# Optimization experiments

Hardware: AMD Instinct MI355X
Metric: run time of the kernel (lower is better)

## Reference

```python
import jax, jax.numpy as jnp
import numpy as np

EMBED = 1024
HEADS = 16
HEAD_DIM = EMBED // HEADS
GROUP_SIZE = 64
NUM_GROUPS = EMBED // GROUP_SIZE
BATCH, SEQ = 2, 2048


def dequantize(qw, scales, zeros):
    # qw: [O, I] int, scales/zeros: [O, NUM_GROUPS]
    O, I = qw.shape
    w = qw.reshape(O, NUM_GROUPS, GROUP_SIZE).astype(scales.dtype)
    w = (w - zeros[:, :, None]) * scales[:, :, None]
    return w.reshape(O, I)


def setup_inputs() -> dict:
    key = jax.random.key(0)
    ks = jax.random.split(key, 17)
    d = {"hidden_states": jax.random.normal(ks[0], (BATCH, SEQ, EMBED), jnp.float32)}
    i = 1
    for p in ("q", "k", "v", "o"):
        d[f"{p}_qw"] = jax.random.randint(ks[i], (EMBED, EMBED), 0, 127, jnp.int32)
        d[f"{p}_scales"] = jax.random.uniform(ks[i + 1], (EMBED, NUM_GROUPS), jnp.float32) * 0.01 + 1e-4
        d[f"{p}_zeros"] = jax.random.uniform(ks[i + 2], (EMBED, NUM_GROUPS), jnp.float32) * 64.0
        d[f"{p}_bias"] = jax.random.normal(ks[i + 3], (EMBED,), jnp.float32) * 0.01
        i += 4
    return d


def reference(hidden_states,
              q_qw, q_scales, q_zeros, q_bias,
              k_qw, k_scales, k_zeros, k_bias,
              v_qw, v_scales, v_zeros, v_bias,
              o_qw, o_scales, o_zeros, o_bias):
    B, S, E = hidden_states.shape

    def proj(x, qw, s, z, b):
        w = dequantize(qw, s, z)  # [O, I]
        return jnp.einsum('bse,oe->bso', x, w) + b

    # [B, S, E] -> [B, H, S, D]
    def split_heads(t):
        return t.reshape(B, S, HEADS, HEAD_DIM).transpose(0, 2, 1, 3)

    q = split_heads(proj(hidden_states, q_qw, q_scales, q_zeros, q_bias))
    k = split_heads(proj(hidden_states, k_qw, k_scales, k_zeros, k_bias))
    v = split_heads(proj(hidden_states, v_qw, v_scales, v_zeros, v_bias))

    scores = jnp.einsum('bhsd,bhtd->bhst', q, k) / (HEAD_DIM ** 0.5)
    attn_weights = jax.nn.softmax(scores, axis=-1)
    attn_out = jnp.einsum('bhst,bhtd->bhsd', attn_weights, v)
    attn_out = attn_out.transpose(0, 2, 1, 3).reshape(B, S, E)

    output = proj(attn_out, o_qw, o_scales, o_zeros, o_bias)
    return output, attn_weights
```

## Files before the change

kernel.cpp:

```cpp
#include <hip/hip_runtime.h>
#include <math.h>

#define EMB 1024
#define NH 16
#define HD 64
#define NB 2
#define SQ 2048
#define BSQ (NB*SQ)
#define NG 16
#define OUT0 ((size_t)BSQ*EMB)

typedef __attribute__((ext_vector_type(8))) short bf16x8;
typedef __attribute__((ext_vector_type(4))) float f32x4;

__device__ __forceinline__ short f2bf(float x){
    unsigned u = __float_as_uint(x);
    u += 0x7fff + ((u >> 16) & 1);
    return (short)(u >> 16);
}
__device__ __forceinline__ float bf2f(short h){
    return __uint_as_float(((unsigned)(unsigned short)h) << 16);
}

__global__ __launch_bounds__(256) void prep_w(
        const int* qq, const float* qs, const float* qz,
        const int* kq, const float* ks, const float* kz,
        const int* vq, const float* vs, const float* vz,
        const int* oq, const float* os, const float* oz,
        short* __restrict__ Wh, short* __restrict__ Wl)
{
    int z = blockIdx.z;
    const int*   qw = z==0?qq : z==1?kq : z==2?vq : oq;
    const float* sc = z==0?qs : z==1?ks : z==2?vs : os;
    const float* zp = z==0?qz : z==1?kz : z==2?vz : oz;
    size_t base = (size_t)z*EMB*EMB;
    int idx = (blockIdx.x*256 + threadIdx.x)*8;
    int4 a = *(const int4*)(qw + idx);
    int4 b = *(const int4*)(qw + idx + 4);
    int o = idx >> 10, g = (idx & 1023) >> 6;
    float s = sc[o*NG + g], zv = zp[o*NG + g];
    int qv[8] = {a.x,a.y,a.z,a.w,b.x,b.y,b.z,b.w};
    alignas(16) short hv[8];
    alignas(16) short lv[8];
    #pragma unroll
    for (int j = 0; j < 8; ++j) {
        float wv = ((float)qv[j] - zv)*s;
        short h = f2bf(wv); hv[j] = h;
        lv[j] = f2bf(wv - bf2f(h));
    }
    *(bf16x8*)(Wh + base + idx) = *(const bf16x8*)hv;
    if (z < 2)
        *(bf16x8*)(Wl + base + idx) = *(const bf16x8*)lv;
}

__global__ __launch_bounds__(256) void prep_x(
        const float* __restrict__ X, short* __restrict__ Xh, short* __restrict__ Xl)
{
    int idx = (blockIdx.x*256 + threadIdx.x)*8;
    float4 a = *(const float4*)(X + idx);
    float4 b = *(const float4*)(X + idx + 4);
    float xv[8] = {a.x,a.y,a.z,a.w,b.x,b.y,b.z,b.w};
    alignas(16) short hv[8];
    alignas(16) short lv[8];
    #pragma unroll
    for (int j = 0; j < 8; ++j) {
        short h = f2bf(xv[j]); hv[j] = h;
        lv[j] = f2bf(xv[j] - bf2f(h));
    }
    *(bf16x8*)(Xh + idx) = *(const bf16x8*)hv;
    *(bf16x8*)(Xl + idx) = *(const bf16x8*)lv;
}

template<int TERMS, int EPI>
__global__ __launch_bounds__(256, 2) void k_proj(
        const short* __restrict__ Ahg, const short* __restrict__ Alg,
        const short* __restrict__ Bhg, const short* __restrict__ Blg,
        const float* __restrict__ bias,
        short* __restrict__ outH, short* __restrict__ outL,
        float* __restrict__ outF)
{
    constexpr bool SPL = (TERMS > 1);
    constexpr int LSTR = 40;
    constexpr int MSZ  = 128*LSTR*(SPL?2:1);
    constexpr int STAGE = 2*MSZ;
    constexpr int TSH  = (EPI == 3) ? 128*136 : 0;
    constexpr int LDSN = (STAGE > TSH) ? STAGE : TSH;
    __shared__ short lds[LDSN];
    short* As  = lds;
    short* Bs  = lds + MSZ;
    short* Asl = As + 128*LSTR;
    short* Bsl = Bs + 128*LSTR;

    const int tid = threadIdx.x;
    const int l = tid & 63, w = tid >> 6;
    const int lrow = l & 15, lq = l >> 4;
    const int wr = w >> 1, wc = w & 1;
    const int m0 = blockIdx.y*128, n0 = blockIdx.x*128;
    const int r = tid >> 1, kh = (tid & 1)*16;

    f32x4 acc[4][4] = {};

    for (int k0 = 0; k0 < EMB; k0 += 32) {
        const short* as = Ahg + (size_t)(m0 + r)*EMB + k0 + kh;
        bf16x8 a0 = *(const bf16x8*)as;
        bf16x8 a1 = *(const bf16x8*)(as + 8);
        const short* bs = Bhg + (size_t)(n0 + r)*EMB + k0 + kh;
        bf16x8 b0 = *(const bf16x8*)bs;
        bf16x8 b1 = *(const bf16x8*)(bs + 8);
        bf16x8 a2{}, a3{}, b2{}, b3{};
        if constexpr (SPL) {
            const short* as2 = Alg + (size_t)(m0 + r)*EMB + k0 + kh;
            a2 = *(const bf16x8*)as2; a3 = *(const bf16x8*)(as2 + 8);
            const short* bs2 = Blg + (size_t)(n0 + r)*EMB + k0 + kh;
            b2 = *(const bf16x8*)bs2; b3 = *(const bf16x8*)(bs2 + 8);
        }
        __syncthreads();
        *(bf16x8*)(As + r*LSTR + kh)     = a0;
        *(bf16x8*)(As + r*LSTR + kh + 8) = a1;
        *(bf16x8*)(Bs + r*LSTR + kh)     = b0;
        *(bf16x8*)(Bs + r*LSTR + kh + 8) = b1;
        if constexpr (SPL) {
            *(bf16x8*)(Asl + r*LSTR + kh)     = a2;
            *(bf16x8*)(Asl + r*LSTR + kh + 8) = a3;
            *(bf16x8*)(Bsl + r*LSTR + kh)     = b2;
            *(bf16x8*)(Bsl + r*LSTR + kh + 8) = b3;
        }
        __syncthreads();

        bf16x8 aH[4], aL[4], bH[4], bL[4];
        #pragma unroll
        for (int i = 0; i < 4; ++i) {
            aH[i] = *(const bf16x8*)(As + (wr*64 + i*16 + lrow)*LSTR + lq*8);
            if constexpr (SPL) aL[i] = *(const bf16x8*)(Asl + (wr*64 + i*16 + lrow)*LSTR + lq*8);
        }
        #pragma unroll
        for (int j = 0; j < 4; ++j) {
            bH[j] = *(const bf16x8*)(Bs + (wc*64 + j*16 + lrow)*LSTR + lq*8);
            if constexpr (SPL) bL[j] = *(const bf16x8*)(Bsl + (wc*64 + j*16 + lrow)*LSTR + lq*8);
        }
        #pragma unroll
        for (int i = 0; i < 4; ++i)
            #pragma unroll
            for (int j = 0; j < 4; ++j) {
                acc[i][j] = __builtin_amdgcn_mfma_f32_16x16x32_bf16(aH[i], bH[j], acc[i][j], 0, 0, 0);
                if constexpr (SPL) {
                    acc[i][j] = __builtin_amdgcn_mfma_f32_16x16x32_bf16(aH[i], bL[j], acc[i][j], 0, 0, 0);
                    acc[i][j] = __builtin_amdgcn_mfma_f32_16x16x32_bf16(aL[i], bH[j], acc[i][j], 0, 0, 0);
                }
            }
    }

    if constexpr (EPI == 3) {
        __syncthreads();
        #pragma unroll
        for (int i = 0; i < 4; ++i) {
            int rl = wr*64 + i*16 + lq*4;
            #pragma unroll
            for (int j = 0; j < 4; ++j) {
                int cl = wc*64 + j*16 + lrow;
                float bv = bias[n0 + cl];
                #pragma unroll
                for (int rr = 0; rr < 4; ++rr)
                    lds[cl*136 + rl + rr] = f2bf(acc[i][j][rr] + bv);
            }
        }
        __syncthreads();
        int c = tid >> 1, hf = (tid & 1)*64;
        int gc = n0 + c;
        int z2 = (m0 >> 11)*16 + (gc >> 6);
        int d = gc & 63;
        short* dst = outH + ((size_t)z2*HD + d)*SQ + (m0 & (SQ-1)) + hf;
        #pragma unroll
        for (int u = 0; u < 8; ++u)
            *(bf16x8*)(dst + u*8) = *(const bf16x8*)(lds + c*136 + hf + u*8);
        return;
    }

    #pragma unroll
    for (int i = 0; i < 4; ++i) {
        int rb = m0 + wr*64 + i*16 + lq*4;
        #pragma unroll
        for (int j = 0; j < 4; ++j) {
            int cb = n0 + wc*64 + j*16 + lrow;
            float bv = bias[cb];
            #pragma unroll
            for (int rr = 0; rr < 4; ++rr) {
                float y = acc[i][j][rr] + bv;
                size_t off = (size_t)(rb + rr)*EMB + cb;
                if constexpr (EPI == 0) {
                    short hh = f2bf(y);
                    outH[off] = hh;
                    outL[off] = f2bf(y - bf2f(hh));
                } else {
                    outF[off] = y;
                }
            }
        }
    }
}

template<int PASS>
__global__ __launch_bounds__(256, 2) void k_attn(
        const short* __restrict__ Qh, const short* __restrict__ Ql,
        const short* __restrict__ Kh, const short* __restrict__ Kl,
        const short* __restrict__ Vt,
        float* __restrict__ ml,
        float* __restrict__ attn,
        short* __restrict__ AO)
{
    constexpr int LSTR = 72;
    __shared__ short qbuf[128*LSTR*2];
    __shared__ short kbuf[64*LSTR*2];
    __shared__ short vbuf[(PASS==2) ? 64*LSTR : 8];
    constexpr int QOFF = 128*LSTR;
    constexpr int KOFF = 64*LSTR;

    const int tid = threadIdx.x;
    const int l = tid & 63, w = tid >> 6;
    const int lrow = l & 15, lq = l >> 4;
    const int z = blockIdx.y, b = z >> 4, h = z & 15;
    const int i0 = blockIdx.x*128;
    const size_t qrow0 = (size_t)(b*SQ + i0);
    const size_t zbase = (size_t)z*SQ*SQ;

    {
        int rr = tid >> 1, kh2 = (tid & 1)*32;
        const short* qh = Qh + (qrow0 + rr)*EMB + h*HD + kh2;
        const short* ql = Ql + (qrow0 + rr)*EMB + h*HD + kh2;
        #pragma unroll
        for (int u = 0; u < 4; ++u) {
            *(bf16x8*)(qbuf + rr*LSTR + kh2 + u*8)        = *(const bf16x8*)(qh + u*8);
            *(bf16x8*)(qbuf + QOFF + rr*LSTR + kh2 + u*8) = *(const bf16x8*)(ql + u*8);
        }
    }
    __syncthreads();
    bf16x8 aH[2][2], aL[2][2];
    #pragma unroll
    for (int i = 0; i < 2; ++i)
        #pragma unroll
        for (int ks = 0; ks < 2; ++ks) {
            aH[i][ks] = *(const bf16x8*)(qbuf + (w*32 + i*16 + lrow)*LSTR + ks*32 + lq*8);
            aL[i][ks] = *(const bf16x8*)(qbuf + QOFF + (w*32 + i*16 + lrow)*LSTR + ks*32 + lq*8);
        }

    float m_st[2][4], l_st[2][4];
    #pragma unroll
    for (int i = 0; i < 2; ++i)
        #pragma unroll
        for (int rr = 0; rr < 4; ++rr) {
            if constexpr (PASS == 1) {
                m_st[i][rr] = -INFINITY; l_st[i][rr] = 0.f;
            } else {
                int row = i0 + w*32 + i*16 + lq*4 + rr;
                m_st[i][rr] = ml[(size_t)z*SQ + row];
                l_st[i][rr] = 1.0f / ml[(size_t)NB*NH*SQ + (size_t)z*SQ + row];
            }
        }

    f32x4 oa[2][4] = {};

    for (int j0 = 0; j0 < SQ; j0 += 64) {
        int c = tid >> 2, kh2 = (tid & 3)*16;
        const short* khp = Kh + (size_t)(b*SQ + j0 + c)*EMB + h*HD + kh2;
        const short* klp = Kl + (size_t)(b*SQ + j0 + c)*EMB + h*HD + kh2;
        bf16x8 k0a = *(const bf16x8*)khp;
        bf16x8 k0b = *(const bf16x8*)(khp + 8);
        bf16x8 k1a = *(const bf16x8*)klp;
        bf16x8 k1b = *(const bf16x8*)(klp + 8);
        bf16x8 va{}, vb{};
        if constexpr (PASS == 2) {
            const short* vp = Vt + ((size_t)z*HD + c)*SQ + j0 + kh2;
            va = *(const bf16x8*)vp;
            vb = *(const bf16x8*)(vp + 8);
        }
        __syncthreads();
        *(bf16x8*)(kbuf + c*LSTR + kh2)            = k0a;
        *(bf16x8*)(kbuf + c*LSTR + kh2 + 8)        = k0b;
        *(bf16x8*)(kbuf + KOFF + c*LSTR + kh2)     = k1a;
        *(bf16x8*)(kbuf + KOFF + c*LSTR + kh2 + 8) = k1b;
        if constexpr (PASS == 2) {
            *(bf16x8*)(vbuf + c*LSTR + kh2)     = va;
            *(bf16x8*)(vbuf + c*LSTR + kh2 + 8) = vb;
        }
        __syncthreads();

        f32x4 acc[2][4] = {};
        #pragma unroll
        for (int ks = 0; ks < 2; ++ks) {
            bf16x8 bH[4], bL[4];
            #pragma unroll
            for (int jj = 0; jj < 4; ++jj) {
                bH[jj] = *(const bf16x8*)(kbuf + (jj*16 + lrow)*LSTR + ks*32 + lq*8);
                bL[jj] = *(const bf16x8*)(kbuf + KOFF + (jj*16 + lrow)*LSTR + ks*32 + lq*8);
            }
            #pragma unroll
            for (int i = 0; i < 2; ++i)
                #pragma unroll
                for (int jj = 0; jj < 4; ++jj) {
                    acc[i][jj] = __builtin_amdgcn_mfma_f32_16x16x32_bf16(aH[i][ks], bH[jj], acc[i][jj], 0, 0, 0);
                    acc[i][jj] = __builtin_amdgcn_mfma_f32_16x16x32_bf16(aH[i][ks], bL[jj], acc[i][jj], 0, 0, 0);
                    acc[i][jj] = __builtin_amdgcn_mfma_f32_16x16x32_bf16(aL[i][ks], bH[jj], acc[i][jj], 0, 0, 0);
                }
        }

        #pragma unroll
        for (int i = 0; i < 2; ++i)
            #pragma unroll
            for (int rr = 0; rr < 4; ++rr) {
                if constexpr (PASS == 1) {
                    float tm = -INFINITY;
                    #pragma unroll
                    for (int jj = 0; jj < 4; ++jj) {
                        acc[i][jj][rr] *= 0.125f;
                        tm = fmaxf(tm, acc[i][jj][rr]);
                    }
                    tm = fmaxf(tm, __shfl_xor(tm, 1));
                    tm = fmaxf(tm, __shfl_xor(tm, 2));
                    tm = fmaxf(tm, __shfl_xor(tm, 4));
                    tm = fmaxf(tm, __shfl_xor(tm, 8));
                    float mn = fmaxf(m_st[i][rr], tm);
                    float ps = 0.f;
                    #pragma unroll
                    for (int jj = 0; jj < 4; ++jj) ps += __expf(acc[i][jj][rr] - mn);
                    ps += __shfl_xor(ps, 1);
                    ps += __shfl_xor(ps, 2);
                    ps += __shfl_xor(ps, 4);
                    ps += __shfl_xor(ps, 8);
                    l_st[i][rr] = l_st[i][rr]*__expf(m_st[i][rr] - mn) + ps;
                    m_st[i][rr] = mn;
                } else {
                    int row = i0 + w*32 + i*16 + lq*4 + rr;
                    #pragma unroll
                    for (int jj = 0; jj < 4; ++jj) {
                        float p = __expf(acc[i][jj][rr]*0.125f - m_st[i][rr]) * l_st[i][rr];
                        attn[zbase + (size_t)row*SQ + j0 + jj*16 + lrow] = p;
                        qbuf[(w*32 + i*16 + lq*4 + rr)*LSTR + jj*16 + lrow] = f2bf(p);
                    }
                }
            }

        if constexpr (PASS == 2) {
            __syncthreads();
            #pragma unroll
            for (int ks = 0; ks < 2; ++ks) {
                bf16x8 ap[2], bv[4];
                #pragma unroll
                for (int i = 0; i < 2; ++i)
                    ap[i] = *(const bf16x8*)(qbuf + (w*32 + i*16 + lrow)*LSTR + ks*32 + lq*8);
                #pragma unroll
                for (int nd = 0; nd < 4; ++nd)
                    bv[nd] = *(const bf16x8*)(vbuf + (nd*16 + lrow)*LSTR + ks*32 + lq*8);
                #pragma unroll
                for (int i = 0; i < 2; ++i)
                    #pragma unroll
                    for (int nd = 0; nd < 4; ++nd)
                        oa[i][nd] = __builtin_amdgcn_mfma_f32_16x16x32_bf16(ap[i], bv[nd], oa[i][nd], 0, 0, 0);
            }
        }
    }

    if constexpr (PASS == 1) {
        if (lrow == 0) {
            #pragma unroll
            for (int i = 0; i < 2; ++i)
                #pragma unroll
                for (int rr = 0; rr < 4; ++rr) {
                    int row = i0 + w*32 + i*16 + lq*4 + rr;
                    ml[(size_t)z*SQ + row] = m_st[i][rr];
                    ml[(size_t)NB*NH*SQ + (size_t)z*SQ + row] = l_st[i][rr];
                }
        }
    } else {
        #pragma unroll
        for (int i = 0; i < 2; ++i)
            #pragma unroll
            for (int rr = 0; rr < 4; ++rr) {
                int row = i0 + w*32 + i*16 + lq*4 + rr;
                #pragma unroll
                for (int nd = 0; nd < 4; ++nd)
                    AO[(size_t)(b*SQ + row)*EMB + h*HD + nd*16 + lrow] = f2bf(oa[i][nd][rr]);
            }
    }
}

extern "C" void kernel_launch(void* const* d_in, const int* in_sizes, int n_in,
                              void* d_out, int out_size, void* d_ws, size_t ws_size,
                              hipStream_t stream)
{
    const float* hs   = (const float*)d_in[0];
    const int*   q_qw = (const int*)  d_in[1];
    const float* q_sc = (const float*)d_in[2];
    const float* q_zp = (const float*)d_in[3];
    const float* q_b  = (const float*)d_in[4];
    const int*   k_qw = (const int*)  d_in[5];
    const float* k_sc = (const float*)d_in[6];
    const float* k_zp = (const float*)d_in[7];
    const float* k_b  = (const float*)d_in[8];
    const int*   v_qw = (const int*)  d_in[9];
    const float* v_sc = (const float*)d_in[10];
    const float* v_zp = (const float*)d_in[11];
    const float* v_b  = (const float*)d_in[12];
    const int*   o_qw = (const int*)  d_in[13];
    const float* o_sc = (const float*)d_in[14];
    const float* o_zp = (const float*)d_in[15];
    const float* o_b  = (const float*)d_in[16];

    float* out  = (float*)d_out;
    float* attn = out + OUT0;

    const size_t WSZ = (size_t)EMB*EMB;
    const size_t TSZ = (size_t)BSQ*EMB;
    float* ml = (float*)d_ws;
    short* Wh = (short*)(ml + 2*(size_t)NB*NH*SQ);
    short* Wl = Wh + 4*WSZ;
    short* Xh = Wl + 2*WSZ;
    short* Xl = Xh + TSZ;
    short* Qh = Xl + TSZ;
    short* Ql = Qh + TSZ;
    short* Kh = Ql + TSZ;
    short* Kl = Kh + TSZ;
    short* Vt = Xl;
    short* AO = Xh;

    dim3 blk(256);

    prep_w<<<dim3(512, 1, 4), blk, 0, stream>>>(
        q_qw, q_sc, q_zp, k_qw, k_sc, k_zp,
        v_qw, v_sc, v_zp, o_qw, o_sc, o_zp, Wh, Wl);
    prep_x<<<dim3(2048), blk, 0, stream>>>(hs, Xh, Xl);

    k_proj<3,0><<<dim3(8,32), blk, 0, stream>>>(Xh, Xl, Wh,       Wl,       q_b, Qh, Ql, nullptr);
    k_proj<3,0><<<dim3(8,32), blk, 0, stream>>>(Xh, Xl, Wh + WSZ, Wl + WSZ, k_b, Kh, Kl, nullptr);
    k_proj<1,3><<<dim3(8,32), blk, 0, stream>>>(Xh, nullptr, Wh + 2*WSZ, nullptr, v_b, Vt, nullptr, nullptr);

    k_attn<1><<<dim3(16,32), blk, 0, stream>>>(Qh, Ql, Kh, Kl, nullptr, ml, nullptr, nullptr);
    k_attn<2><<<dim3(16,32), blk, 0, stream>>>(Qh, Ql, Kh, Kl, Vt, ml, attn, AO);

    k_proj<1,2><<<dim3(8,32), blk, 0, stream>>>(AO, nullptr, Wh + 3*WSZ, nullptr, o_b, nullptr, nullptr, out);
}
```

Before: 898.1 us.

## Merge prep and QK launches, defer softmax stat reduction, use nontemporal stores

Folds the weight and activation prep into one launch and the Q/K projections into one launch using a z grid dimension. In pass 1 of attention, each lane keeps its own running max/sum, and the cross-lane shuffle merge is done once at the end instead of every key tile. Pass 2 drops a __syncthreads before the P·V step, relying on each wave reading only the rows it wrote. The large attention-probability and final outputs use nontemporal stores to cut cache pollution. The removed barrier risks a race if vbuf or qbuf visibility depended on it.

Result: faster. 820.8 us (-8.6%).

```diff
diff --git a/kernel.cpp b/kernel.cpp
--- a/kernel.cpp
+++ b/kernel.cpp
@@ -22,62 +22,61 @@
     return __uint_as_float(((unsigned)(unsigned short)h) << 16);
 }
 
-__global__ __launch_bounds__(256) void prep_w(
+__global__ __launch_bounds__(256) void k_prep(
+        const float* __restrict__ hs,
         const int* qq, const float* qs, const float* qz,
         const int* kq, const float* ks, const float* kz,
         const int* vq, const float* vs, const float* vz,
         const int* oq, const float* os, const float* oz,
-        short* __restrict__ Wh, short* __restrict__ Wl)
+        short* __restrict__ Wh, short* __restrict__ Wl,
+        short* __restrict__ Xh, short* __restrict__ Xl)
 {
     int z = blockIdx.z;
-    const int*   qw = z==0?qq : z==1?kq : z==2?vq : oq;
-    const float* sc = z==0?qs : z==1?ks : z==2?vs : os;
-    const float* zp = z==0?qz : z==1?kz : z==2?vz : oz;
-    size_t base = (size_t)z*EMB*EMB;
     int idx = (blockIdx.x*256 + threadIdx.x)*8;
-    int4 a = *(const int4*)(qw + idx);
-    int4 b = *(const int4*)(qw + idx + 4);
-    int o = idx >> 10, g = (idx & 1023) >> 6;
-    float s = sc[o*NG + g], zv = zp[o*NG + g];
-    int qv[8] = {a.x,a.y,a.z,a.w,b.x,b.y,b.z,b.w};
     alignas(16) short hv[8];
     alignas(16) short lv[8];
-    #pragma unroll
-    for (int j = 0; j < 8; ++j) {
-        float wv = ((float)qv[j] - zv)*s;
-        short h = f2bf(wv); hv[j] = h;
-        lv[j] = f2bf(wv - bf2f(h));
-    }
-    *(bf16x8*)(Wh + base + idx) = *(const bf16x8*)hv;
-    if (z < 2)
-        *(bf16x8*)(Wl + base + idx) = *(const bf16x8*)lv;
-}
-
-__global__ __launch_bounds__(256) void prep_x(
-        const float* __restrict__ X, short* __restrict__ Xh, short* __restrict__ Xl)
-{
-    int idx = (blockIdx.x*256 + threadIdx.x)*8;
-    float4 a = *(const float4*)(X + idx);
-    float4 b = *(const float4*)(X + idx + 4);
-    float xv[8] = {a.x,a.y,a.z,a.w,b.x,b.y,b.z,b.w};
-    alignas(16) short hv[8];
-    alignas(16) short lv[8];
-    #pragma unroll
-    for (int j = 0; j < 8; ++j) {
-        short h = f2bf(xv[j]); hv[j] = h;
-        lv[j] = f2bf(xv[j] - bf2f(h));
-    }
-    *(bf16x8*)(Xh + idx) = *(const bf16x8*)hv;
-    *(bf16x8*)(Xl + idx) = *(const bf16x8*)lv;
+    if (z < 4) {
+        const int*   qw = z==0?qq : z==1?kq : z==2?vq : oq;
+        const float* sc = z==0?qs : z==1?ks : z==2?vs : os;
+        const float* zp = z==0?qz : z==1?kz : z==2?vz : oz;
+        size_t base = (size_t)z*EMB*EMB;
+        int4 a = *(const int4*)(qw + idx);
+        int4 b = *(const int4*)(qw + idx + 4);
+        int o = idx >> 10, g = (idx & 1023) >> 6;
+        float s = sc[o*NG + g], zv = zp[o*NG + g];
+        int qv[8] = {a.x,a.y,a.z,a.w,b.x,b.y,b.z,b.w};
+        #pragma unroll
+        for (int j = 0; j < 8; ++j) {
+            float wv = ((float)qv[j] - zv)*s;
+            short h = f2bf(wv); hv[j] = h;
+            lv[j] = f2bf(wv - bf2f(h));
+        }
+        *(bf16x8*)(Wh + base + idx) = *(const bf16x8*)hv;
+        if (z < 2)
+            *(bf16x8*)(Wl + base + idx) = *(const bf16x8*)lv;
+    } else {
+        size_t off = (size_t)(z - 4)*((size_t)BSQ/4*EMB) + idx;
+        float4 a = *(const float4*)(hs + off);
+        float4 b = *(const float4*)(hs + off + 4);
+        float xv[8] = {a.x,a.y,a.z,a.w,b.x,b.y,b.z,b.w};
+        #pragma unroll
+        for (int j = 0; j < 8; ++j) {
+            short h = f2bf(xv[j]); hv[j] = h;
+            lv[j] = f2bf(xv[j] - bf2f(h));
+        }
+        *(bf16x8*)(Xh + off) = *(const bf16x8*)hv;
+        *(bf16x8*)(Xl + off) = *(const bf16x8*)lv;
+    }
 }
 
 template<int TERMS, int EPI>
-__global__ __launch_bounds__(256, 2) void k_proj(
+__device__ __forceinline__ void proj_body(
         const short* __restrict__ Ahg, const short* __restrict__ Alg,
         const short* __restrict__ Bhg, const short* __restrict__ Blg,
         const float* __restrict__ bias,
         short* __restrict__ outH, short* __restrict__ outL,
-        float* __restrict__ outF)
+        float* __restrict__ outF,
+        int bx, int by)
 {
     constexpr bool SPL = (TERMS > 1);
     constexpr int LSTR = 40;
@@ -95,7 +94,7 @@
     const int l = tid & 63, w = tid >> 6;
     const int lrow = l & 15, lq = l >> 4;
     const int wr = w >> 1, wc = w & 1;
-    const int m0 = blockIdx.y*128, n0 = blockIdx.x*128;
+    const int m0 = by*128, n0 = bx*128;
     const int r = tid >> 1, kh = (tid & 1)*16;
 
     f32x4 acc[4][4] = {};
@@ -192,11 +191,40 @@
                     outH[off] = hh;
                     outL[off] = f2bf(y - bf2f(hh));
                 } else {
-                    outF[off] = y;
-                }
-            }
-        }
-    }
+                    __builtin_nontemporal_store(y, outF + off);
+                }
+            }
+        }
+    }
+}
+
+__global__ __launch_bounds__(256, 2) void k_projqk(
+        const short* __restrict__ Xh, const short* __restrict__ Xl,
+        const short* __restrict__ Wh, const short* __restrict__ Wl,
+        const float* bq, const float* bk,
+        short* Qh, short* Ql, short* Kh, short* Kl)
+{
+    const size_t WSZ = (size_t)EMB*EMB;
+    int z = blockIdx.z;
+    proj_body<3,0>(Xh, Xl, Wh + (size_t)z*WSZ, Wl + (size_t)z*WSZ,
+                   z ? bk : bq, z ? Kh : Qh, z ? Kl : Ql, nullptr,
+                   blockIdx.x, blockIdx.y);
+}
+
+__global__ __launch_bounds__(256, 2) void k_projv(
+        const short* __restrict__ Xh, const short* __restrict__ Wh,
+        const float* bv, short* Vt)
+{
+    proj_body<1,3>(Xh, nullptr, Wh, nullptr, bv, Vt, nullptr, nullptr,
+                   blockIdx.x, blockIdx.y);
+}
+
+__global__ __launch_bounds__(256, 2) void k_projo(
+        const short* __restrict__ AO, const short* __restrict__ Wh,
+        const float* bo, float* out)
+{
+    proj_body<1,2>(AO, nullptr, Wh, nullptr, bo, nullptr, nullptr, out,
+                   blockIdx.x, blockIdx.y);
 }
 
 template<int PASS>
@@ -308,39 +336,29 @@
             #pragma unroll
             for (int rr = 0; rr < 4; ++rr) {
                 if constexpr (PASS == 1) {
-                    float tm = -INFINITY;
-                    #pragma unroll
-                    for (int jj = 0; jj < 4; ++jj) {
-                        acc[i][jj][rr] *= 0.125f;
-                        tm = fmaxf(tm, acc[i][jj][rr]);
-                    }
-                    tm = fmaxf(tm, __shfl_xor(tm, 1));
-                    tm = fmaxf(tm, __shfl_xor(tm, 2));
-                    tm = fmaxf(tm, __shfl_xor(tm, 4));
-                    tm = fmaxf(tm, __shfl_xor(tm, 8));
-                    float mn = fmaxf(m_st[i][rr], tm);
-                    float ps = 0.f;
-                    #pragma unroll
-                    for (int jj = 0; jj < 4; ++jj) ps += __expf(acc[i][jj][rr] - mn);
-                    ps += __shfl_xor(ps, 1);
-                    ps += __shfl_xor(ps, 2);
-                    ps += __shfl_xor(ps, 4);
-                    ps += __shfl_xor(ps, 8);
-                    l_st[i][rr] = l_st[i][rr]*__expf(m_st[i][rr] - mn) + ps;
+                    float s0 = acc[i][0][rr]*0.125f;
+                    float s1 = acc[i][1][rr]*0.125f;
+                    float s2 = acc[i][2][rr]*0.125f;
+                    float s3 = acc[i][3][rr]*0.125f;
+                    float tm = fmaxf(fmaxf(s0, s1), fmaxf(s2, s3));
+                    float mo = m_st[i][rr];
+                    float mn = fmaxf(mo, tm);
+                    l_st[i][rr] = l_st[i][rr]*__expf(mo - mn)
+                                + __expf(s0 - mn) + __expf(s1 - mn)
+                                + __expf(s2 - mn) + __expf(s3 - mn);
                     m_st[i][rr] = mn;
                 } else {
                     int row = i0 + w*32 + i*16 + lq*4 + rr;
                     #pragma unroll
                     for (int jj = 0; jj < 4; ++jj) {
                         float p = __expf(acc[i][jj][rr]*0.125f - m_st[i][rr]) * l_st[i][rr];
-                        attn[zbase + (size_t)row*SQ + j0 + jj*16 + lrow] = p;
+                        __builtin_nontemporal_store(p, attn + zbase + (size_t)row*SQ + j0 + jj*16 + lrow);
                         qbuf[(w*32 + i*16 + lq*4 + rr)*LSTR + jj*16 + lrow] = f2bf(p);
                     }
                 }
             }
 
         if constexpr (PASS == 2) {
-            __syncthreads();
             #pragma unroll
             for (int ks = 0; ks < 2; ++ks) {
                 bf16x8 ap[2], bv[4];
@@ -360,16 +378,25 @@
     }
 
     if constexpr (PASS == 1) {
-        if (lrow == 0) {
-            #pragma unroll
-            for (int i = 0; i < 2; ++i)
-                #pragma unroll
-                for (int rr = 0; rr < 4; ++rr) {
+        #pragma unroll
+        for (int i = 0; i < 2; ++i)
+            #pragma unroll
+            for (int rr = 0; rr < 4; ++rr) {
+                float m = m_st[i][rr], lv = l_st[i][rr];
+                #pragma unroll
+                for (int off = 1; off < 16; off <<= 1) {
+                    float m2 = __shfl_xor(m, off);
+                    float l2 = __shfl_xor(lv, off);
+                    float mn = fmaxf(m, m2);
+                    lv = lv*__expf(m - mn) + l2*__expf(m2 - mn);
+                    m = mn;
+                }
+                if (lrow == 0) {
                     int row = i0 + w*32 + i*16 + lq*4 + rr;
-                    ml[(size_t)z*SQ + row] = m_st[i][rr];
-                    ml[(size_t)NB*NH*SQ + (size_t)z*SQ + row] = l_st[i][rr];
-                }
-        }
+                    ml[(size_t)z*SQ + row] = m;
+                    ml[(size_t)NB*NH*SQ + (size_t)z*SQ + row] = lv;
+                }
+            }
     } else {
         #pragma unroll
         for (int i = 0; i < 2; ++i)
@@ -424,17 +451,19 @@
 
     dim3 blk(256);
 
-    prep_w<<<dim3(512, 1, 4), blk, 0, stream>>>(
+    k_prep<<<dim3(512, 1, 8), blk, 0, stream>>>(
+        hs,
         q_qw, q_sc, q_zp, k_qw, k_sc, k_zp,
-        v_qw, v_sc, v_zp, o_qw, o_sc, o_zp, Wh, Wl);
-    prep_x<<<dim3(2048), blk, 0, stream>>>(hs, Xh, Xl);
-
-    k_proj<3,0><<<dim3(8,32), blk, 0, stream>>>(Xh, Xl, Wh,       Wl,       q_b, Qh, Ql, nullptr);
-    k_proj<3,0><<<dim3(8,32), blk, 0, stream>>>(Xh, Xl, Wh + WSZ, Wl + WSZ, k_b, Kh, Kl, nullptr);
-    k_proj<1,3><<<dim3(8,32), blk, 0, stream>>>(Xh, nullptr, Wh + 2*WSZ, nullptr, v_b, Vt, nullptr, nullptr);
-
-    k_attn<1><<<dim3(16,32), blk, 0, stream>>>(Qh, Ql, Kh, Kl, nullptr, ml, nullptr, nullptr);
-    k_attn<2><<<dim3(16,32), blk, 0, stream>>>(Qh, Ql, Kh, Kl, Vt, ml, attn, AO);
-
-    k_proj<1,2><<<dim3(8,32), blk, 0, stream>>>(AO, nullptr, Wh + 3*WSZ, nullptr, o_b, nullptr, nullptr, out);
-}
+        v_qw, v_sc, v_zp, o_qw, o_sc, o_zp,
+        Wh, Wl, Xh, Xl);
+
+    k_projqk<<<dim3(8, 32, 2), blk, 0, stream>>>(
+        Xh, Xl, Wh, Wl, q_b, k_b, Qh, Ql, Kh, Kl);
+
+    k_projv<<<dim3(8, 32), blk, 0, stream>>>(Xh, Wh + 2*WSZ, v_b, Vt);
+
+    k_attn<1><<<dim3(16, 32), blk, 0, stream>>>(Qh, Ql, Kh, Kl, nullptr, ml, nullptr, nullptr);
+    k_attn<2><<<dim3(16, 32), blk, 0, stream>>>(Qh, Ql, Kh, Kl, Vt, ml, attn, AO);
+
+    k_projo<<<dim3(8, 32), blk, 0, stream>>>(AO, Wh + 3*WSZ, o_b, out);
+}
```
